# Kernel optimization log

Hardware: AMD Instinct MI355X
Metric: run time of the kernel (lower is better)

## Reference

```python
import jax, jax.numpy as jnp
import numpy as np

NUM_EXPERTS = 8
TOP_K = 2
RANK = 16
LORA_ALPHA = 32
SCALING = LORA_ALPHA / RANK  # 2.0


def setup_inputs() -> dict:
    key = jax.random.key(0)
    ks = jax.random.split(key, 6)
    B, S, D_IN, D_OUT = 4, 2048, 4096, 4096
    x = jax.random.normal(ks[0], (B, S, D_IN), dtype=jnp.float32)
    W_base = jax.random.normal(ks[1], (D_OUT, D_IN), dtype=jnp.float32) * 0.02
    b_base = jax.random.normal(ks[2], (D_OUT,), dtype=jnp.float32) * 0.02
    W_router = jax.random.normal(ks[3], (NUM_EXPERTS, D_IN), dtype=jnp.float32) * 0.02
    A = jax.random.normal(ks[4], (NUM_EXPERTS, RANK, D_IN), dtype=jnp.float32) * 0.02
    Bm = jax.random.normal(ks[5], (D_OUT, RANK), dtype=jnp.float32) * 0.02
    Bm = jnp.broadcast_to(Bm, (NUM_EXPERTS, D_OUT, RANK)) * jnp.arange(1, NUM_EXPERTS + 1, dtype=jnp.float32)[:, None, None] * 0.2
    return {"x": x, "W_base": W_base, "b_base": b_base, "W_router": W_router, "A": A, "B": Bm}


def reference(x, W_base, b_base, W_router, A, B):
    bs, seq, d_in = x.shape
    T = bs * seq
    xf = x.reshape(T, d_in)  # flatten tokens, as in torch .view(-1, d_in)

    # base linear layer
    base = xf @ W_base.T + b_base  # [T, d_out]

    # local router: logits -> top-k -> softmax over selected weights
    logits = xf @ W_router.T                      # [T, E]
    rw, sel = jax.lax.top_k(logits, TOP_K)        # [T, K] each
    rw = jax.nn.softmax(rw, axis=-1)              # router_norm == 'softmax'

    # per-token per-expert combine weight (zero for unselected experts);
    # mathematically identical to gather-LoRA-scatter since top-k experts
    # per token are distinct.
    onehot = jax.nn.one_hot(sel, NUM_EXPERTS, dtype=rw.dtype)  # [T, K, E]
    w = jnp.einsum('tk,tke->te', rw, onehot)                   # [T, E]

    # LoRA: down-project to tiny rank, weight, then up-project; contract
    # expert+rank together to avoid a [T, E, d_out] intermediate.
    h = jnp.einsum('td,erd->ter', xf, A)          # [T, E, r] (small)
    lora = jnp.einsum('ter,te,eor->to', h, w, B) * SCALING  # [T, d_out]

    return (base + lora).reshape(bs, seq, -1)
```

## Files before the change

kernel.cpp:

```cpp
#include <hip/hip_runtime.h>
#include <hip/hip_bf16.h>
#include <stdint.h>

#define T_TOKENS 8192
#define DIN      4096
#define DOUT     4096
#define NE       8
#define RANK     16
#define KEXT     128
#define KTOT     4224
#define NT       66
#define SCALING  2.0f

typedef __attribute__((ext_vector_type(8))) short   short8;
typedef __attribute__((ext_vector_type(4))) float   float4v;

__device__ __forceinline__ unsigned short f2bf(float f) {
    union { float f; unsigned int u; } c; c.f = f;
    unsigned int u = c.u;
    u += 0x7FFFu + ((u >> 16) & 1u);
    return (unsigned short)(u >> 16);
}

#define GLD_LDS(g, l) __builtin_amdgcn_global_load_lds( \
    (const __attribute__((address_space(1))) void*)(g), \
    (__attribute__((address_space(3))) void*)(l), 16, 0, 0)

__global__ __launch_bounds__(256) void k_front(const float* __restrict__ x,
                                               const float* __restrict__ Wr,
                                               const float* __restrict__ Wb,
                                               const float* __restrict__ A,
                                               const float* __restrict__ Bm,
                                               unsigned short* __restrict__ xa,
                                               unsigned short* __restrict__ Wa,
                                               unsigned short* __restrict__ Acat,
                                               float* __restrict__ w8) {
    __shared__ float lds_wr[8 * 1024];
    int b = blockIdx.x;
    int tid = threadIdx.x;

    if (b < 2048) {
        int l = tid & 63, w = tid >> 6;
        int t = b * 4 + w;
        const float4* x4 = (const float4*)x;
        const float4* Wr4 = (const float4*)Wr;
        unsigned short* xarow = xa + (size_t)t * KTOT;

        float racc[NE];
#pragma unroll
        for (int e = 0; e < NE; e++) racc[e] = 0.f;

        for (int ci = 0; ci < 4; ci++) {
            __syncthreads();
#pragma unroll
            for (int jj = 0; jj < 8; jj++) {
                int f = jj * 256 + tid;
                int e = f >> 8, col = f & 255;
                *(float4*)&lds_wr[f * 4] = Wr4[e * 1024 + ci * 256 + col];
            }
            __syncthreads();
            float4 xv[4];
#pragma unroll
            for (int j = 0; j < 4; j++)
                xv[j] = x4[(size_t)t * 1024 + ci * 256 + j * 64 + l];
#pragma unroll
            for (int j = 0; j < 4; j++) {
                ushort4 p;
                p.x = f2bf(xv[j].x); p.y = f2bf(xv[j].y);
                p.z = f2bf(xv[j].z); p.w = f2bf(xv[j].w);
                *(ushort4*)(xarow + (ci * 256 + j * 64 + l) * 4) = p;
            }
#pragma unroll
            for (int e = 0; e < NE; e++) {
#pragma unroll
                for (int j = 0; j < 4; j++) {
                    float4 wv = *(const float4*)&lds_wr[(e * 256 + j * 64 + l) * 4];
                    racc[e] += xv[j].x * wv.x + xv[j].y * wv.y + xv[j].z * wv.z + xv[j].w * wv.w;
                }
            }
        }
#pragma unroll
        for (int e = 0; e < NE; e++) {
            float v = racc[e];
#pragma unroll
            for (int off = 32; off > 0; off >>= 1) v += __shfl_xor(v, off);
            racc[e] = v;
        }
        if (l == 0) {
            int e0 = 0;
#pragma unroll
            for (int e = 1; e < NE; e++) if (racc[e] > racc[e0]) e0 = e;
            int e1 = -1;
#pragma unroll
            for (int e = 0; e < NE; e++)
                if (e != e0 && (e1 < 0 || racc[e] > racc[e1])) e1 = e;
            float a1 = __expf(racc[e1] - racc[e0]);
            float inv = 1.0f / (1.0f + a1);
            float* wrow = w8 + t * NE;
#pragma unroll
            for (int e = 0; e < NE; e++)
                wrow[e] = (e == e0) ? inv * SCALING : ((e == e1) ? a1 * inv * SCALING : 0.f);
        }
    } else if (b < 18432) {
        int idx = (b - 2048) * 256 + tid;
        float4 v = ((const float4*)Wb)[idx];
        int o  = idx >> 10;
        int kc = idx & 1023;
        ushort4 p;
        p.x = f2bf(v.x); p.y = f2bf(v.y); p.z = f2bf(v.z); p.w = f2bf(v.w);
        *(ushort4*)(Wa + (size_t)o * KTOT + kc * 4) = p;
    } else {
        int tid2 = (b - 18432) * 256 + tid;
        if (tid2 < NE * RANK * DIN) {
            Acat[tid2] = f2bf(A[tid2]);
        } else {
            int j   = tid2 - NE * RANK * DIN;
            int o   = j >> 7;
            int rem = j & 127;
            int e   = rem >> 4;
            int r   = rem & 15;
            Wa[(size_t)o * KTOT + DIN + rem] = f2bf(Bm[(size_t)e * (DOUT * RANK) + o * RANK + r]);
        }
    }
}

__global__ __launch_bounds__(256) void k_h(unsigned short* __restrict__ xa,
                                           const unsigned short* __restrict__ Acat,
                                           const float* __restrict__ w8) {
    __shared__ unsigned short lds_x[32 * 128];
    __shared__ unsigned short lds_a[128 * 128];
    int m0  = blockIdx.x * 32;
    int tid = threadIdx.x;
    int l = tid & 63, w = tid >> 6;
    int quad = l >> 4, lr = l & 15;

    float4v acc[2][2] = {};

    for (int k0 = 0; k0 < DIN; k0 += 128) {
        __syncthreads();
#pragma unroll
        for (int it = 0; it < 2; it++) {
            int c = it * 256 + tid;
            int row = c >> 4, s = c & 15;
            int kc = s ^ (row & 15);
            GLD_LDS(xa + (size_t)(m0 + row) * KTOT + k0 + kc * 8, lds_x + c * 8);
        }
#pragma unroll
        for (int it = 0; it < 8; it++) {
            int c = it * 256 + tid;
            int row = c >> 4, s = c & 15;
            int kc = s ^ (row & 15);
            GLD_LDS(Acat + (size_t)row * DIN + k0 + kc * 8, lds_a + c * 8);
        }
        __syncthreads();
#pragma unroll
        for (int kk = 0; kk < 4; kk++) {
            int kc = kk * 4 + quad;
            short8 a[2], bfr[2];
#pragma unroll
            for (int mi = 0; mi < 2; mi++) {
                int row = mi * 16 + lr;
                a[mi] = *(const short8*)&lds_x[row * 128 + ((kc ^ lr) * 8)];
            }
#pragma unroll
            for (int ni = 0; ni < 2; ni++) {
                int row = w * 32 + ni * 16 + lr;
                bfr[ni] = *(const short8*)&lds_a[row * 128 + ((kc ^ lr) * 8)];
            }
#pragma unroll
            for (int mi = 0; mi < 2; mi++)
#pragma unroll
                for (int ni = 0; ni < 2; ni++)
                    acc[mi][ni] = __builtin_amdgcn_mfma_f32_16x16x32_bf16(a[mi], bfr[ni], acc[mi][ni], 0, 0, 0);
        }
    }

#pragma unroll
    for (int mi = 0; mi < 2; mi++)
#pragma unroll
        for (int ni = 0; ni < 2; ni++) {
            int col = w * 32 + ni * 16 + lr;
            int e = col >> 4;
#pragma unroll
            for (int i = 0; i < 4; i++) {
                int t = m0 + mi * 16 + quad * 4 + i;
                float v = acc[mi][ni][i] * w8[t * NE + e];
                xa[(size_t)t * KTOT + DIN + col] = f2bf(v);
            }
        }
}

#define LOADA(dst, basep, mlo) { \
    _Pragma("unroll") for (int i_ = 0; i_ < 4; i_++) \
        dst[i_] = *(const short8*)((basep) + aoff + ((mlo) + i_) * 1024); }
#define LOADB(dst, basep) { \
    _Pragma("unroll") for (int i_ = 0; i_ < 4; i_++) \
        dst[i_] = *(const short8*)((basep) + boff + i_ * 1024); }
#define MFMA44(mlo) { \
    __builtin_amdgcn_s_setprio(1); \
    _Pragma("unroll") for (int i_ = 0; i_ < 4; i_++) \
    _Pragma("unroll") for (int j_ = 0; j_ < 4; j_++) \
        acc[(mlo) + i_][j_] = __builtin_amdgcn_mfma_f32_16x16x32_bf16(af[i_], bf[j_], acc[(mlo) + i_][j_], 0, 0, 0); \
    __builtin_amdgcn_s_setprio(0); }
#define STAGE(srcP, regbase, ts, kh, tb) do { \
    const unsigned short* s_ = (srcP) + (size_t)((ts) * 64 + (kh) * 32); \
    char* d_ = smem + (regbase) + (tb) * 32768 + (kh) * 16384 + tid16; \
    GLD_LDS(s_, d_); \
    GLD_LDS(s_ + (size_t)128 * KTOT, d_ + 8192); \
} while (0)
#define BAR() __builtin_amdgcn_s_barrier()
#define LGKM0() do { asm volatile("s_waitcnt lgkmcnt(0)" ::: "memory"); \
                     __builtin_amdgcn_sched_barrier(0); } while (0)

__global__ __launch_bounds__(512, 2) void k_main(const unsigned short* __restrict__ xa,
                                                 const unsigned short* __restrict__ Wa,
                                                 const float* __restrict__ bias,
                                                 float* __restrict__ out) {
    extern __shared__ char smem[];
    int tid = threadIdx.x;
    int l = tid & 63, w = tid >> 6;
    int lr = l & 15, quad = l >> 4;
    int wm = w >> 2, wn = w & 3;

    int bid = blockIdx.x;
    int wg  = (bid & 7) * 64 + (bid >> 3);
    int bm  = wg & 31, bn = wg >> 5;

    int laneoff = (lr * 4 + (quad ^ ((lr >> 1) & 3))) * 16;
    int aoff = wm * 8192 + laneoff;
    int boff = wn * 4096 + laneoff;

    int srow  = w * 16 + ((tid >> 2) & 15);
    int skq   = (tid & 3) ^ ((tid >> 3) & 3);
    int tid16 = tid * 16;
    const unsigned short* srcA = xa + (size_t)(bm * 256 + srow) * KTOT + skq * 8;
    const unsigned short* srcB = Wa + (size_t)(bn * 256 + srow) * KTOT + skq * 8;

    float4v acc[8][4] = {};
    short8 af[4], bf[4];

    STAGE(srcA, 0,     0, 0, 0);
    STAGE(srcB, 65536, 0, 0, 0);
    STAGE(srcA, 0,     0, 1, 0);
    STAGE(srcB, 65536, 0, 1, 0);
    STAGE(srcA, 0,     1, 0, 1);
    STAGE(srcB, 65536, 1, 0, 1);
    asm volatile("s_waitcnt vmcnt(4)" ::: "memory");
    BAR();

    for (int t = 0; t < NT; ++t) {
        int buf  = t & 1, nbuf = buf ^ 1;
        int ts1  = (t + 1 < NT) ? t + 1 : NT - 1;
        int ts2  = (t + 2 < NT) ? t + 2 : NT - 1;
        const char* pa = smem + buf * 32768;
        const char* pb = smem + 65536 + buf * 32768;

        LOADA(af, pa, 0);
        LOADB(bf, pb);
        STAGE(srcA, 0, ts1, 1, nbuf);
        BAR(); LGKM0();
        MFMA44(0);
        BAR();

        LOADA(af, pa, 4);
        STAGE(srcB, 65536, ts1, 1, nbuf);
        BAR(); LGKM0();
        MFMA44(4);
        BAR();

        LOADA(af, pa + 16384, 0);
        LOADB(bf, pb + 16384);
        STAGE(srcA, 0, ts2, 0, buf);
        BAR(); LGKM0();
        MFMA44(0);
        BAR();

        LOADA(af, pa + 16384, 4);
        STAGE(srcB, 65536, ts2, 0, buf);
        asm volatile("s_waitcnt vmcnt(4)" ::: "memory");
        BAR(); LGKM0();
        MFMA44(4);
        BAR();
    }

    int trow0 = bm * 256 + wm * 128;
    int ocol0 = bn * 256 + wn * 64;
#pragma unroll
    for (int ni = 0; ni < 4; ni++) {
        int o = ocol0 + ni * 16 + lr;
        float bb = bias[o];
#pragma unroll
        for (int mi = 0; mi < 8; mi++) {
#pragma unroll
            for (int i = 0; i < 4; i++) {
                int trow = trow0 + mi * 16 + quad * 4 + i;
                out[(size_t)trow * DOUT + o] = acc[mi][ni][i] + bb;
            }
        }
    }
}

extern "C" void kernel_launch(void* const* d_in, const int* in_sizes, int n_in,
                              void* d_out, int out_size, void* d_ws, size_t ws_size,
                              hipStream_t stream) {
    const float* x  = (const float*)d_in[0];
    const float* Wb = (const float*)d_in[1];
    const float* bb = (const float*)d_in[2];
    const float* Wr = (const float*)d_in[3];
    const float* A  = (const float*)d_in[4];
    const float* Bm = (const float*)d_in[5];
    float* out = (float*)d_out;

    char* ws = (char*)d_ws;
    unsigned short* xa   = (unsigned short*)(ws);
    unsigned short* Wa   = (unsigned short*)(ws + 69206016);
    unsigned short* Acat = (unsigned short*)(ws + 69206016 + 34603008);
    float*          w8   = (float*)(ws + 69206016 + 34603008 + 1048576);

    static bool attr_done = false;
    if (!attr_done) {
        hipFuncSetAttribute((const void*)k_main,
                            hipFuncAttributeMaxDynamicSharedMemorySize, 131072);
        attr_done = true;
    }

    k_front<<<dim3(22528), dim3(256), 0, stream>>>(x, Wr, Wb, A, Bm, xa, Wa, Acat, w8);
    k_h    <<<dim3(256),   dim3(256), 0, stream>>>(xa, Acat, w8);
    k_main <<<dim3(512),   dim3(512), 131072, stream>>>(xa, Wa, bb, out);
}
```

Baseline: 571.3 us.

## Vectorize front conversions, drop router LDS staging, double-buffer k_h loads

```diff
diff --git a/kernel.cpp b/kernel.cpp
--- a/kernel.cpp
+++ b/kernel.cpp
@@ -35,7 +35,6 @@
                                                unsigned short* __restrict__ Wa,
                                                unsigned short* __restrict__ Acat,
                                                float* __restrict__ w8) {
-    __shared__ float lds_wr[8 * 1024];
     int b = blockIdx.x;
     int tid = threadIdx.x;
 
@@ -50,33 +49,17 @@
 #pragma unroll
         for (int e = 0; e < NE; e++) racc[e] = 0.f;
 
-        for (int ci = 0; ci < 4; ci++) {
-            __syncthreads();
-#pragma unroll
-            for (int jj = 0; jj < 8; jj++) {
-                int f = jj * 256 + tid;
-                int e = f >> 8, col = f & 255;
-                *(float4*)&lds_wr[f * 4] = Wr4[e * 1024 + ci * 256 + col];
-            }
-            __syncthreads();
-            float4 xv[4];
-#pragma unroll
-            for (int j = 0; j < 4; j++)
-                xv[j] = x4[(size_t)t * 1024 + ci * 256 + j * 64 + l];
-#pragma unroll
-            for (int j = 0; j < 4; j++) {
-                ushort4 p;
-                p.x = f2bf(xv[j].x); p.y = f2bf(xv[j].y);
-                p.z = f2bf(xv[j].z); p.w = f2bf(xv[j].w);
-                *(ushort4*)(xarow + (ci * 256 + j * 64 + l) * 4) = p;
-            }
+#pragma unroll 4
+        for (int ci = 0; ci < 16; ci++) {
+            float4 xv = x4[(size_t)t * 1024 + ci * 64 + l];
+            ushort4 p;
+            p.x = f2bf(xv.x); p.y = f2bf(xv.y);
+            p.z = f2bf(xv.z); p.w = f2bf(xv.w);
+            *(ushort4*)(xarow + (ci * 64 + l) * 4) = p;
 #pragma unroll
             for (int e = 0; e < NE; e++) {
-#pragma unroll
-                for (int j = 0; j < 4; j++) {
-                    float4 wv = *(const float4*)&lds_wr[(e * 256 + j * 64 + l) * 4];
-                    racc[e] += xv[j].x * wv.x + xv[j].y * wv.y + xv[j].z * wv.z + xv[j].w * wv.w;
-                }
+                float4 wv = Wr4[e * 1024 + ci * 64 + l];
+                racc[e] += xv.x * wv.x + xv.y * wv.y + xv.z * wv.z + xv.w * wv.w;
             }
         }
 #pragma unroll
@@ -101,34 +84,61 @@
             for (int e = 0; e < NE; e++)
                 wrow[e] = (e == e0) ? inv * SCALING : ((e == e1) ? a1 * inv * SCALING : 0.f);
         }
-    } else if (b < 18432) {
-        int idx = (b - 2048) * 256 + tid;
-        float4 v = ((const float4*)Wb)[idx];
-        int o  = idx >> 10;
-        int kc = idx & 1023;
-        ushort4 p;
-        p.x = f2bf(v.x); p.y = f2bf(v.y); p.z = f2bf(v.z); p.w = f2bf(v.w);
-        *(ushort4*)(Wa + (size_t)o * KTOT + kc * 4) = p;
+    } else if (b < 6144) {
+        int base = (b - 2048) * 1024 + tid;
+#pragma unroll
+        for (int j = 0; j < 4; j++) {
+            int idx = base + j * 256;
+            float4 v = ((const float4*)Wb)[idx];
+            int o  = idx >> 10;
+            int kc = idx & 1023;
+            ushort4 p;
+            p.x = f2bf(v.x); p.y = f2bf(v.y); p.z = f2bf(v.z); p.w = f2bf(v.w);
+            *(ushort4*)(Wa + (size_t)o * KTOT + kc * 4) = p;
+        }
     } else {
-        int tid2 = (b - 18432) * 256 + tid;
-        if (tid2 < NE * RANK * DIN) {
-            Acat[tid2] = f2bf(A[tid2]);
+        int idx = (b - 6144) * 256 + tid;
+        if (idx < 131072) {
+            float4 v = ((const float4*)A)[idx];
+            ushort4 p;
+            p.x = f2bf(v.x); p.y = f2bf(v.y); p.z = f2bf(v.z); p.w = f2bf(v.w);
+            *(ushort4*)(Acat + (size_t)idx * 4) = p;
         } else {
-            int j   = tid2 - NE * RANK * DIN;
-            int o   = j >> 7;
-            int rem = j & 127;
-            int e   = rem >> 4;
-            int r   = rem & 15;
-            Wa[(size_t)o * KTOT + DIN + rem] = f2bf(Bm[(size_t)e * (DOUT * RANK) + o * RANK + r]);
-        }
-    }
-}
+            int j = idx - 131072;
+            int o = j >> 5;
+            int q = j & 31;
+            int e = q >> 2;
+            float4 v = ((const float4*)Bm)[(size_t)e * 16384 + o * 4 + (q & 3)];
+            ushort4 p;
+            p.x = f2bf(v.x); p.y = f2bf(v.y); p.z = f2bf(v.z); p.w = f2bf(v.w);
+            *(ushort4*)(Wa + (size_t)o * KTOT + DIN + q * 4) = p;
+        }
+    }
+}
+
+#define STAGEH(kt, bb) do { \
+    int k0_ = (kt) * 128; \
+    _Pragma("unroll") \
+    for (int it_ = 0; it_ < 2; it_++) { \
+        int c_ = it_ * 256 + tid; \
+        int row_ = c_ >> 4, s_ = c_ & 15; \
+        int kc_ = s_ ^ (row_ & 15); \
+        GLD_LDS(xa + (size_t)(m0 + row_) * KTOT + k0_ + kc_ * 8, lds_x + (bb) * 4096 + c_ * 8); \
+    } \
+    _Pragma("unroll") \
+    for (int it_ = 0; it_ < 8; it_++) { \
+        int c_ = it_ * 256 + tid; \
+        int row_ = c_ >> 4, s_ = c_ & 15; \
+        int kc_ = s_ ^ (row_ & 15); \
+        GLD_LDS(Acat + (size_t)row_ * DIN + k0_ + kc_ * 8, lds_a + (bb) * 16384 + c_ * 8); \
+    } \
+} while (0)
 
 __global__ __launch_bounds__(256) void k_h(unsigned short* __restrict__ xa,
                                            const unsigned short* __restrict__ Acat,
                                            const float* __restrict__ w8) {
-    __shared__ unsigned short lds_x[32 * 128];
-    __shared__ unsigned short lds_a[128 * 128];
+    __shared__ unsigned short lds_x[2 * 32 * 128];
+    __shared__ unsigned short lds_a[2 * 128 * 128];
     int m0  = blockIdx.x * 32;
     int tid = threadIdx.x;
     int l = tid & 63, w = tid >> 6;
@@ -136,23 +146,18 @@
 
     float4v acc[2][2] = {};
 
-    for (int k0 = 0; k0 < DIN; k0 += 128) {
+    STAGEH(0, 0);
+    for (int kt = 0; kt < 32; ++kt) {
+        int bb = kt & 1;
+        if (kt + 1 < 32) {
+            STAGEH(kt + 1, bb ^ 1);
+            asm volatile("s_waitcnt vmcnt(10)" ::: "memory");
+        } else {
+            asm volatile("s_waitcnt vmcnt(0)" ::: "memory");
+        }
         __syncthreads();
-#pragma unroll
-        for (int it = 0; it < 2; it++) {
-            int c = it * 256 + tid;
-            int row = c >> 4, s = c & 15;
-            int kc = s ^ (row & 15);
-            GLD_LDS(xa + (size_t)(m0 + row) * KTOT + k0 + kc * 8, lds_x + c * 8);
-        }
-#pragma unroll
-        for (int it = 0; it < 8; it++) {
-            int c = it * 256 + tid;
-            int row = c >> 4, s = c & 15;
-            int kc = s ^ (row & 15);
-            GLD_LDS(Acat + (size_t)row * DIN + k0 + kc * 8, lds_a + c * 8);
-        }
-        __syncthreads();
+        const unsigned short* lx = lds_x + bb * 4096;
+        const unsigned short* la = lds_a + bb * 16384;
 #pragma unroll
         for (int kk = 0; kk < 4; kk++) {
             int kc = kk * 4 + quad;
@@ -160,12 +165,12 @@
 #pragma unroll
             for (int mi = 0; mi < 2; mi++) {
                 int row = mi * 16 + lr;
-                a[mi] = *(const short8*)&lds_x[row * 128 + ((kc ^ lr) * 8)];
+                a[mi] = *(const short8*)&lx[row * 128 + ((kc ^ lr) * 8)];
             }
 #pragma unroll
             for (int ni = 0; ni < 2; ni++) {
                 int row = w * 32 + ni * 16 + lr;
-                bfr[ni] = *(const short8*)&lds_a[row * 128 + ((kc ^ lr) * 8)];
+                bfr[ni] = *(const short8*)&la[row * 128 + ((kc ^ lr) * 8)];
             }
 #pragma unroll
             for (int mi = 0; mi < 2; mi++)
@@ -173,6 +178,7 @@
                 for (int ni = 0; ni < 2; ni++)
                     acc[mi][ni] = __builtin_amdgcn_mfma_f32_16x16x32_bf16(a[mi], bfr[ni], acc[mi][ni], 0, 0, 0);
         }
+        __syncthreads();
     }
 
 #pragma unroll
@@ -324,7 +330,7 @@
         attr_done = true;
     }
 
-    k_front<<<dim3(22528), dim3(256), 0, stream>>>(x, Wr, Wb, A, Bm, xa, Wa, Acat, w8);
+    k_front<<<dim3(7168),  dim3(256), 0, stream>>>(x, Wr, Wb, A, Bm, xa, Wa, Acat, w8);
     k_h    <<<dim3(256),   dim3(256), 0, stream>>>(xa, Acat, w8);
     k_main <<<dim3(512),   dim3(512), 131072, stream>>>(xa, Wa, bb, out);
 }
```

Measured after the change: 592.2 us. 3.7% more time.
